# Performance work log

Measured on AMD Instinct MI355X. Metric: run time of the kernel, lower is better.

Reference implementation:

```python
import jax, jax.numpy as jnp
import numpy as np


def _gcn_norm(edge_index, edge_weight, n_nodes):
    # PyG gcn_norm with add_self_loops=True, fill_value=1.0.
    row, col = edge_index[0], edge_index[1]
    loop = jnp.arange(n_nodes, dtype=edge_index.dtype)
    row = jnp.concatenate([row, loop])
    col = jnp.concatenate([col, loop])
    w = jnp.concatenate([edge_weight, jnp.ones((n_nodes,), edge_weight.dtype)])
    deg = jax.ops.segment_sum(w, col, num_segments=n_nodes)
    dinv = jnp.where(deg > 0, jax.lax.rsqrt(deg), 0.0)
    norm = dinv[row] * w * dinv[col]
    return row, col, norm


def _gcn_conv(x, row, col, norm, W, b, n_nodes):
    h = x @ W                                  # [N, F_out]
    msg = h[row] * norm[:, None]               # gather + scale, [E+N, F_out]
    out = jax.ops.segment_sum(msg, col, num_segments=n_nodes)
    return out + b


def setup_inputs() -> dict:
    key = jax.random.key(0)
    k = jax.random.split(key, 7)
    N, E, Fin, Fout = 50000, 1600000, 256, 128
    H = 2 * Fout
    x = jax.random.normal(k[0], (N, Fin), dtype=jnp.float32)
    edge_index = jax.random.randint(k[1], (2, E), 0, N, dtype=jnp.int64)
    edge_weight = jax.random.uniform(k[2], (E,), dtype=jnp.float32)
    # Glorot init as in PyG GCNConv (weight stored as [in, out] here)
    s1 = float(np.sqrt(6.0 / (Fin + H)))
    s2 = float(np.sqrt(6.0 / (H + Fout)))
    W1 = jax.random.uniform(k[3], (Fin, H), minval=-s1, maxval=s1, dtype=jnp.float32)
    b1 = jnp.zeros((H,), jnp.float32)
    W2 = jax.random.uniform(k[4], (H, Fout), minval=-s2, maxval=s2, dtype=jnp.float32)
    b2 = jnp.zeros((Fout,), jnp.float32)
    return {"x": x, "edge_index": edge_index, "edge_weight": edge_weight,
            "W1": W1, "b1": b1, "W2": W2, "b2": b2}


def reference(x, edge_index, edge_weight, W1, b1, W2, b2):
    n_nodes = x.shape[0]
    # cached=True: normalization computed once, reused by both layers
    row, col, norm = _gcn_norm(edge_index, edge_weight, n_nodes)
    h = _gcn_conv(x, row, col, norm, W1, b1, n_nodes)
    h = jax.nn.relu(h)
    out = _gcn_conv(h, row, col, norm, W2, b2, n_nodes)
    return out
```

## Files before the change

### kernel.cpp

```cpp
#include <hip/hip_runtime.h>

typedef __attribute__((ext_vector_type(8))) short  short8;
typedef __attribute__((ext_vector_type(4))) float  f32x4;
typedef __attribute__((ext_vector_type(4))) ushort us4;
typedef __attribute__((ext_vector_type(4))) uint   u32x4;
typedef __attribute__((ext_vector_type(2))) uint   u32x2;
typedef unsigned long long ull;

__device__ __forceinline__ float bf2f(ushort u) {
    union { uint i; float f; } c; c.i = ((uint)u) << 16; return c.f;
}
__device__ __forceinline__ float bits2f(uint b) {
    union { uint i; float f; } c; c.i = b; return c.f;
}
__device__ __forceinline__ ushort f2bf(float f) {
    union { float f; uint i; } c; c.f = f;
    uint b = c.i + 0x7fffu + ((c.i >> 16) & 1u);
    return (ushort)(b >> 16);
}

#define NBLK  256
#define NBMAX 1024

__device__ __forceinline__
void histA_body(const int* __restrict__ col, int* __restrict__ counts,
                int E, int NB, uint* hist) {
    for (int j = threadIdx.x; j < NB; j += 256) hist[j] = 0u;
    __syncthreads();
    for (int i = blockIdx.x * 256 + threadIdx.x; i < E; i += 256 * NBLK)
        atomicAdd(&hist[((uint)col[i]) >> 6], 1u);
    __syncthreads();
    for (int j = threadIdx.x; j < NB; j += 256)
        counts[j * NBLK + blockIdx.x] = (int)hist[j];
}

__device__ __forceinline__
void binC_body(const int* __restrict__ row, const int* __restrict__ col,
               const float* __restrict__ w,
               const int* __restrict__ counts, const int* __restrict__ bbase,
               ull* __restrict__ recs, int E, int NB, uint* cur) {
    for (int j = threadIdx.x; j < NB; j += 256)
        cur[j] = (uint)(bbase[j] + counts[j * NBLK + blockIdx.x]);
    __syncthreads();
    for (int i = blockIdx.x * 256 + threadIdx.x; i < E; i += 256 * NBLK) {
        int c = col[i], r = row[i];
        float wv = w[i];
        uint w16 = (uint)(wv * 65536.0f);
        if (w16 > 65535u) w16 = 65535u;
        uint pos = atomicAdd(&cur[((uint)c) >> 6], 1u);
        recs[pos] = ((ull)(uint)c << 32) | (ull)((w16 << 16) | (uint)(r & 0xffff));
    }
}

__device__ __forceinline__
void binDa_body(const ull* __restrict__ recs, const int* __restrict__ bbase,
                int* __restrict__ cntp, float* __restrict__ dinv,
                int* __restrict__ btotP, int N,
                uint* cnt, uint* ws, uint* red) {
    int b = blockIdx.x, t = threadIdx.x;
    if (t < 64) { cnt[t] = 0u; ws[t] = 0u; }
    __syncthreads();
    int lo = bbase[b], hi = bbase[b + 1];
    for (int i = lo + t; i < hi; i += 256) {
        ull rec = recs[i];
        atomicAdd(&cnt[((uint)(rec >> 32)) & 63u], 1u);
        atomicAdd(&ws[((uint)(rec >> 32)) & 63u], (uint)((rec >> 16) & 0xffffu));
    }
    __syncthreads();
    uint cp = 0;
    if (t < 64) {
        int node = b * 64 + t;
        if (node < N) {
            cp = (cnt[t] + 3u) & ~3u;
            cntp[node] = (int)cp;
            dinv[node] = rsqrtf(1.0f + (float)ws[t] * (1.0f / 65536.0f));
        }
        red[t] = cp;
    }
    __syncthreads();
    if (t < 32) red[t] += red[t + 32];
    __syncthreads();
    if (t < 16) red[t] += red[t + 16];
    __syncthreads();
    if (t < 8) red[t] += red[t + 8];
    __syncthreads();
    if (t < 4) red[t] += red[t + 4];
    __syncthreads();
    if (t == 0) btotP[b] = (int)(red[0] + red[1] + red[2] + red[3]);
}

__device__ __forceinline__
void binDb_body(const ull* __restrict__ recs, const int* __restrict__ bbase,
                const int* __restrict__ bbaseP, const int* __restrict__ cntp,
                const float* __restrict__ dinv, int* __restrict__ rowptr,
                uint* __restrict__ edgesP, int N,
                uint* arr, uint* curN, uint* rbs) {
    int b = blockIdx.x, t = threadIdx.x;
    int node = b * 64 + t;
    uint cp = 0;
    if (t < 64 && node < N) cp = (uint)cntp[node];
    if (t < 64) arr[t] = cp;
    __syncthreads();
    for (int off = 1; off < 64; off <<= 1) {
        uint x = (t < 64 && t >= off) ? arr[t - off] : 0u;
        __syncthreads();
        if (t < 64) arr[t] += x;
        __syncthreads();
    }
    if (t < 64) {
        uint rb = (uint)bbaseP[b] + arr[t] - cp;
        rbs[t] = rb; curN[t] = rb;
        if (node < N) rowptr[node] = (int)rb;
    }
    __syncthreads();
    int lo = bbase[b], hi = bbase[b + 1];
    for (int i = lo + t; i < hi; i += 256) {
        ull rec = recs[i];
        uint c   = (uint)(rec >> 32);
        uint r   = (uint)rec & 0xffffu;
        uint w16 = ((uint)rec >> 16) & 0xffffu;
        float nv = dinv[r] * ((float)w16 * (1.0f / 65536.0f)) * dinv[c];
        uint slot = atomicAdd(&curN[c & 63u], 1u);
        edgesP[slot] = r | ((uint)f2bf(nv) << 16);
    }
    __syncthreads();
    if (t < 64 && node < N) {
        uint e1 = rbs[t] + cp;
        for (uint j = curN[t]; j < e1; ++j) edgesP[j] = 0u;
    }
}

__global__ void k_scanB1(int* __restrict__ counts, int* __restrict__ btot) {
    __shared__ int s[256];
    int b = blockIdx.x, t = threadIdx.x;
    int v = counts[b * NBLK + t];
    s[t] = v; __syncthreads();
    for (int off = 1; off < 256; off <<= 1) {
        int x = (t >= off) ? s[t - off] : 0;
        __syncthreads();
        s[t] += x;
        __syncthreads();
    }
    counts[b * NBLK + t] = s[t] - v;
    if (t == 255) btot[b] = s[255];
}

__global__ void k_scanB2(const int* __restrict__ btot, int* __restrict__ bbase, int NB) {
    __shared__ int s[256];
    int t = threadIdx.x;
    int v[4]; int sum = 0;
    #pragma unroll
    for (int j = 0; j < 4; ++j) {
        int i = t * 4 + j;
        v[j] = (i < NB) ? btot[i] : 0;
        sum += v[j];
    }
    s[t] = sum; __syncthreads();
    for (int off = 1; off < 256; off <<= 1) {
        int x = (t >= off) ? s[t - off] : 0;
        __syncthreads();
        s[t] += x;
        __syncthreads();
    }
    int excl = s[t] - sum;
    #pragma unroll
    for (int j = 0; j < 4; ++j) {
        int i = t * 4 + j;
        if (i <= NB) bbase[i] = excl;
        excl += v[j];
    }
}

__device__ __forceinline__
void splitT_body(const float* __restrict__ W, ushort* __restrict__ Th,
                 ushort* __restrict__ Tl, int K, int N, int i) {
    if (i < K * N) {
        int k = i / N, n = i - k * N;
        float v = W[i];
        ushort hi = f2bf(v);
        ushort lo = f2bf(v - bf2f(hi));
        Th[(size_t)n * K + k] = hi;
        Tl[(size_t)n * K + k] = lo;
    }
}

#define LDA 40

__device__ __forceinline__
void gemm3_body(const float* __restrict__ A, const ushort* __restrict__ BTh,
                const ushort* __restrict__ BTl, ushort* __restrict__ Cpan,
                int M, int Nc, int K, int bm, int bn,
                ushort (*As)[128][LDA], ushort (*Bs)[128][LDA]) {
    const int t    = threadIdx.x;
    const int lane = t & 63;
    const int wid  = t >> 6;
    const int wm   = wid >> 1;
    const int wn   = wid & 1;
    const int ml   = lane & 15;
    const int kq   = lane >> 4;

    f32x4 acc[4][4];
    #pragma unroll
    for (int mt = 0; mt < 4; ++mt)
        #pragma unroll
        for (int nt = 0; nt < 4; ++nt) acc[mt][nt] = (f32x4){0.f, 0.f, 0.f, 0.f};

    for (int k0 = 0; k0 < K; k0 += 32) {
        #pragma unroll
        for (int it = 0; it < 4; ++it) {
            int idx = (t + it * 256) * 4;
            int r  = idx >> 5;
            int kk = idx & 31;
            int grow = bm + r;
            f32x4 v = (f32x4){0.f, 0.f, 0.f, 0.f};
            if (grow < M) v = *(const f32x4*)&A[(size_t)grow * K + k0 + kk];
            us4 hi, lo;
            #pragma unroll
            for (int j = 0; j < 4; ++j) {
                ushort h = f2bf(v[j]);
                hi[j] = h;
                lo[j] = f2bf(v[j] - bf2f(h));
            }
            *(us4*)&As[0][r][kk] = hi;
            *(us4*)&As[1][r][kk] = lo;
        }
        #pragma unroll
        for (int it = 0; it < 2; ++it) {
            int idx = (t + it * 256) * 8;
            int n  = idx >> 5;
            int kk = idx & 31;
            u32x4 vh = *(const u32x4*)&BTh[(size_t)(bn + n) * K + k0 + kk];
            *(u32x4*)&Bs[0][n][kk] = vh;
            u32x4 vl = *(const u32x4*)&BTl[(size_t)(bn + n) * K + k0 + kk];
            *(u32x4*)&Bs[1][n][kk] = vl;
        }
        __syncthreads();

        short8 a[4][2], b[4][2];
        #pragma unroll
        for (int mt = 0; mt < 4; ++mt) {
            a[mt][0] = *(const short8*)&As[0][wm * 64 + mt * 16 + ml][kq * 8];
            a[mt][1] = *(const short8*)&As[1][wm * 64 + mt * 16 + ml][kq * 8];
        }
        #pragma unroll
        for (int nt = 0; nt < 4; ++nt) {
            b[nt][0] = *(const short8*)&Bs[0][wn * 64 + nt * 16 + ml][kq * 8];
            b[nt][1] = *(const short8*)&Bs[1][wn * 64 + nt * 16 + ml][kq * 8];
        }
        #pragma unroll
        for (int mt = 0; mt < 4; ++mt)
            #pragma unroll
            for (int nt = 0; nt < 4; ++nt) {
                acc[mt][nt] = __builtin_amdgcn_mfma_f32_16x16x32_bf16(a[mt][0], b[nt][0], acc[mt][nt], 0, 0, 0);
                acc[mt][nt] = __builtin_amdgcn_mfma_f32_16x16x32_bf16(a[mt][0], b[nt][1], acc[mt][nt], 0, 0, 0);
                acc[mt][nt] = __builtin_amdgcn_mfma_f32_16x16x32_bf16(a[mt][1], b[nt][0], acc[mt][nt], 0, 0, 0);
            }
        __syncthreads();
    }

    #pragma unroll
    for (int mt = 0; mt < 4; ++mt) {
        int rbase = bm + wm * 64 + mt * 16 + kq * 4;
        #pragma unroll
        for (int nt = 0; nt < 4; ++nt) {
            int colg = bn + wn * 64 + nt * 16 + ml;
            size_t pbase = (size_t)(colg >> 5) * M * 32 + (colg & 31);
            #pragma unroll
            for (int r = 0; r < 4; ++r) {
                int rr = rbase + r;
                if (rr < M) Cpan[pbase + (size_t)rr * 32] = f2bf(acc[mt][nt][r]);
            }
        }
    }
}

__global__ __launch_bounds__(256)
void k_gemm3(const float* __restrict__ A, const ushort* __restrict__ BTh,
             const ushort* __restrict__ BTl, ushort* __restrict__ Cpan,
             int M, int Nc, int K) {
    __shared__ __align__(16) ushort As[2][128][LDA];
    __shared__ __align__(16) ushort Bs[2][128][LDA];
    gemm3_body(A, BTh, BTl, Cpan, M, Nc, K, blockIdx.y * 128, blockIdx.x * 128, As, Bs);
}

__global__ __launch_bounds__(256)
void k_fusedA(const int* __restrict__ col, int* __restrict__ counts, int E, int NB,
              const float* __restrict__ W1, ushort* __restrict__ WT1h, ushort* __restrict__ WT1l,
              int Fin, int H,
              const float* __restrict__ W2, ushort* __restrict__ WT2h, ushort* __restrict__ WT2l,
              int Fout, int sp1) {
    __shared__ uint hist[NBMAX];
    int bid = (int)blockIdx.x;
    if (bid < NBLK) { histA_body(col, counts, E, NB, hist); return; }
    if (bid < NBLK + sp1) { splitT_body(W1, WT1h, WT1l, Fin, H, (bid - NBLK) * 256 + (int)threadIdx.x); return; }
    splitT_body(W2, WT2h, WT2l, H, Fout, (bid - NBLK - sp1) * 256 + (int)threadIdx.x);
}

__global__ __launch_bounds__(256)
void k_fusedB1(const int* __restrict__ row, const int* __restrict__ col,
               const float* __restrict__ w, const int* __restrict__ counts,
               const int* __restrict__ bbase, ull* __restrict__ recs, int E, int NB,
               const float* __restrict__ A, const ushort* __restrict__ BTh,
               const ushort* __restrict__ BTl, ushort* __restrict__ Cpan,
               int M, int Nc, int K, int t0) {
    __shared__ __align__(16) ushort As[2][128][LDA];
    __shared__ __align__(16) ushort Bs[2][128][LDA];
    int bid = (int)blockIdx.x;
    if (bid < NBLK) { binC_body(row, col, w, counts, bbase, recs, E, NB, (uint*)&As[0][0][0]); return; }
    int tile = t0 + bid - NBLK;
    int nbn = Nc >> 7;
    gemm3_body(A, BTh, BTl, Cpan, M, Nc, K, (tile / nbn) * 128, (tile % nbn) * 128, As, Bs);
}

__global__ __launch_bounds__(256)
void k_fusedB2(const ull* __restrict__ recs, const int* __restrict__ bbase,
               int* __restrict__ cntp, float* __restrict__ dinv, int* __restrict__ btotP,
               int N, int NB,
               const float* __restrict__ A, const ushort* __restrict__ BTh,
               const ushort* __restrict__ BTl, ushort* __restrict__ Cpan,
               int M, int Nc, int K, int t0) {
    __shared__ __align__(16) ushort As[2][128][LDA];
    __shared__ __align__(16) ushort Bs[2][128][LDA];
    int bid = (int)blockIdx.x;
    if (bid < NB) {
        uint* l = (uint*)&As[0][0][0];
        binDa_body(recs, bbase, cntp, dinv, btotP, N, l, l + 64, l + 128);
        return;
    }
    int tile = t0 + bid - NB;
    int nbn = Nc >> 7;
    gemm3_body(A, BTh, BTl, Cpan, M, Nc, K, (tile / nbn) * 128, (tile % nbn) * 128, As, Bs);
}

__global__ __launch_bounds__(256)
void k_fusedB3(const ull* __restrict__ recs, const int* __restrict__ bbase,
               const int* __restrict__ bbaseP, const int* __restrict__ cntp,
               const float* __restrict__ dinv, int* __restrict__ rowptr,
               uint* __restrict__ edgesP, int N, int NB,
               const float* __restrict__ A, const ushort* __restrict__ BTh,
               const ushort* __restrict__ BTl, ushort* __restrict__ Cpan,
               int M, int Nc, int K, int t0) {
    __shared__ __align__(16) ushort As[2][128][LDA];
    __shared__ __align__(16) ushort Bs[2][128][LDA];
    int bid = (int)blockIdx.x;
    if (bid < NB) {
        uint* l = (uint*)&As[0][0][0];
        binDb_body(recs, bbase, bbaseP, cntp, dinv, rowptr, edgesP, N, l, l + 64, l + 128);
        return;
    }
    int tile = t0 + bid - NB;
    int nbn = Nc >> 7;
    gemm3_body(A, BTh, BTl, Cpan, M, Nc, K, (tile / nbn) * 128, (tile % nbn) * 128, As, Bs);
}

#define NPB 64

template <bool RELU>
__device__ __forceinline__
void aggr_body(const int* __restrict__ rowptr, const int* __restrict__ cntp,
               const uint* __restrict__ edges,
               const ushort* __restrict__ hpan, const float* __restrict__ dinv,
               const float* __restrict__ bias, float* __restrict__ out,
               int F, int npan, int N) {
    const int bid  = blockIdx.x;
    const int p    = bid % npan;
    const int wave = threadIdx.x >> 6;
    const int lane = threadIdx.x & 63;
    const int g    = lane >> 2;
    const int c    = lane & 3;
    const int node = (bid / npan) * NPB + wave * 16 + g;
    const int fbase = p * 32 + c * 8;

    const ushort* hp = hpan + (size_t)p * N * 32 + c * 8;

    int beg = 0, end = 0;
    if (node < N) { beg = rowptr[node]; end = beg + cntp[node]; }

    float acc[8] = {};
    int e = beg;
    u32x4 pk4 = (u32x4){0u, 0u, 0u, 0u};
    if (e < end) pk4 = *(const u32x4*)&edges[e];
    while (__any(e < end)) {
        u32x4 cur = pk4;
        int e2 = e + 4;
        if (e2 < end) pk4 = *(const u32x4*)&edges[e2];
        if (e < end) {
            #pragma unroll
            for (int j = 0; j < 4; ++j) {
                uint pk = cur[j];
                float nv = bits2f(pk & 0xffff0000u);
                int r = (int)(pk & 0xffffu);
                u32x4 hv = *(const u32x4*)(hp + (size_t)r * 32);
                #pragma unroll
                for (int q = 0; q < 4; ++q) {
                    acc[2 * q]     += nv * bits2f(hv[q] << 16);
                    acc[2 * q + 1] += nv * bits2f(hv[q] & 0xffff0000u);
                }
            }
        }
        e = e2;
    }

    if (node < N) {
        float di = dinv[node];
        float d2 = di * di;
        u32x4 hs = *(const u32x4*)(hp + (size_t)node * 32);
        f32x4 bv0 = *(const f32x4*)&bias[fbase];
        f32x4 bv1 = *(const f32x4*)&bias[fbase + 4];
        f32x4 v0, v1;
        #pragma unroll
        for (int q = 0; q < 4; ++q) {
            float r0 = acc[2 * q]     + d2 * bits2f(hs[q] << 16)
                     + ((q < 2) ? bv0[2 * q] : bv1[2 * q - 4]);
            float r1 = acc[2 * q + 1] + d2 * bits2f(hs[q] & 0xffff0000u)
                     + ((q < 2) ? bv0[2 * q + 1] : bv1[2 * q - 3]);
            if (RELU) { r0 = fmaxf(r0, 0.f); r1 = fmaxf(r1, 0.f); }
            if (q < 2) { v0[2 * q] = r0; v0[2 * q + 1] = r1; }
            else       { v1[2 * q - 4] = r0; v1[2 * q - 3] = r1; }
        }
        *(f32x4*)&out[(size_t)node * F + fbase]     = v0;
        *(f32x4*)&out[(size_t)node * F + fbase + 4] = v1;
    }
}

__global__ __launch_bounds__(256)
void k_aggr1(const int* __restrict__ rowptr, const int* __restrict__ cntp,
             const uint* __restrict__ edges, const ushort* __restrict__ hpan,
             const float* __restrict__ dinv, const float* __restrict__ bias,
             float* __restrict__ out, int F, int npan, int N) {
    aggr_body<true>(rowptr, cntp, edges, hpan, dinv, bias, out, F, npan, N);
}

__global__ __launch_bounds__(256)
void k_aggr2(const int* __restrict__ rowptr, const int* __restrict__ cntp,
             const uint* __restrict__ edges, const ushort* __restrict__ hpan,
             const float* __restrict__ dinv, const float* __restrict__ bias,
             float* __restrict__ out, int F, int npan, int N) {
    aggr_body<false>(rowptr, cntp, edges, hpan, dinv, bias, out, F, npan, N);
}


static inline char* bump(char*& p, size_t bytes) {
    char* r = p;
    p += (bytes + 255) & ~(size_t)255;
    return r;
}

extern "C" void kernel_launch(void* const* d_in, const int* in_sizes, int n_in,
                              void* d_out, int out_size, void* d_ws, size_t ws_size,
                              hipStream_t stream) {
    const float* x  = (const float*)d_in[0];
    const int*   ei = (const int*)d_in[1];
    const float* ew = (const float*)d_in[2];
    const float* W1 = (const float*)d_in[3];
    const float* b1 = (const float*)d_in[4];
    const float* W2 = (const float*)d_in[5];
    const float* b2 = (const float*)d_in[6];
    float* out = (float*)d_out;

    const int E    = in_sizes[2];
    const int H    = in_sizes[4];
    const int Fout = in_sizes[6];
    const int Fin  = in_sizes[3] / H;
    const int N    = in_sizes[0] / Fin;
    const int NB   = (N + 63) >> 6;

    const int* row = ei;
    const int* col = ei + E;

    char* p = (char*)d_ws;
    float*  dinv   = (float*)bump(p, (size_t)N * 4);
    int*    cntp   = (int*)bump(p, (size_t)N * 4);
    int*    rowptr = (int*)bump(p, (size_t)N * 4);
    uint*   edgesP = (uint*)bump(p, ((size_t)E + 4 * N + 256) * 4);
    int*    counts = (int*)bump(p, (size_t)NBMAX * NBLK * 4);
    int*    btot   = (int*)bump(p, (size_t)NBMAX * 4);
    int*    bbase  = (int*)bump(p, (size_t)(NBMAX + 1) * 4);
    int*    btotP  = (int*)bump(p, (size_t)NBMAX * 4);
    int*    bbaseP = (int*)bump(p, (size_t)(NBMAX + 1) * 4);
    ushort* WT1h   = (ushort*)bump(p, (size_t)Fin * H * 2);
    ushort* WT1l   = (ushort*)bump(p, (size_t)Fin * H * 2);
    ushort* WT2h   = (ushort*)bump(p, (size_t)H * Fout * 2);
    ushort* WT2l   = (ushort*)bump(p, (size_t)H * Fout * 2);
    ushort* h1     = (ushort*)bump(p, (size_t)N * H * 2);
    float*  a1     = (float*)bump(p, (size_t)N * H * 4);
    ushort* h2     = (ushort*)bump(p, (size_t)N * Fout * 2);

    ull* recs = (ull*)a1;

    const int sp1 = (Fin * H + 255) / 256;
    const int sp2 = (H * Fout + 255) / 256;
    const int gb1 = (H / 128) * ((N + 127) / 128);
    int T1 = gb1 < 280 ? gb1 : 280;
    int T2 = gb1 < 480 ? gb1 : 480;
    if (T2 < T1) T2 = T1;

    k_fusedA<<<NBLK + sp1 + sp2, 256, 0, stream>>>(col, counts, E, NB,
                                                   W1, WT1h, WT1l, Fin, H,
                                                   W2, WT2h, WT2l, Fout, sp1);
    k_scanB1<<<NB, 256, 0, stream>>>(counts, btot);
    k_scanB2<<<1, 256, 0, stream>>>(btot, bbase, NB);
    k_fusedB1<<<NBLK + T1, 256, 0, stream>>>(row, col, ew, counts, bbase, recs, E, NB,
                                             x, WT1h, WT1l, h1, N, H, Fin, 0);
    k_fusedB2<<<NB + (T2 - T1), 256, 0, stream>>>(recs, bbase, cntp, dinv, btotP, N, NB,
                                                  x, WT1h, WT1l, h1, N, H, Fin, T1);
    k_scanB2<<<1, 256, 0, stream>>>(btotP, bbaseP, NB);
    k_fusedB3<<<NB + (gb1 - T2), 256, 0, stream>>>(recs, bbase, bbaseP, cntp, dinv,
                                                   rowptr, edgesP, N, NB,
                                                   x, WT1h, WT1l, h1, N, H, Fin, T2);

    const int chunks = (N + NPB - 1) / NPB;

    k_aggr1<<<chunks * (H / 32), 256, 0, stream>>>(rowptr, cntp, edgesP, h1, dinv, b1, a1, H, H / 32, N);

    k_gemm3<<<dim3(Fout / 128, (N + 127) / 128), 256, 0, stream>>>(a1, WT2h, WT2l, h2, N, Fout, H);
    k_aggr2<<<chunks * (Fout / 32), 256, 0, stream>>>(rowptr, cntp, edgesP, h2, dinv, b2, out, Fout, Fout / 32, N);
}
```

Baseline: 417.5 us.

## Sort nodes by padded degree for aggregation and drop second per-bin scan

Builds a counting sort of nodes by padded in-degree bucket (histogram, scan, placement into a ushort perm array) and has both aggregation kernels walk nodes in that order. Nodes sharing a wave then have similar edge counts, which cuts divergence and idle lanes. Row pointers are now computed in the degree pass from a fixed per-bin over-allocation (192 slots per bin), so the second block-total scan launch goes away. The cost is extra atomics, a small scan kernel, scattered output writes and lost locality between neighbouring nodes, and the perm indices are limited to 16 bits.

After: 890.1 us. 113% more time.

```diff
diff --git a/kernel.cpp b/kernel.cpp
--- a/kernel.cpp
+++ b/kernel.cpp
@@ -55,8 +55,8 @@
 __device__ __forceinline__
 void binDa_body(const ull* __restrict__ recs, const int* __restrict__ bbase,
                 int* __restrict__ cntp, float* __restrict__ dinv,
-                int* __restrict__ btotP, int N,
-                uint* cnt, uint* ws, uint* red) {
+                int* __restrict__ rowptr, uint* __restrict__ pkhist, int N,
+                uint* cnt, uint* ws, uint* arr) {
     int b = blockIdx.x, t = threadIdx.x;
     if (t < 64) { cnt[t] = 0u; ws[t] = 0u; }
     __syncthreads();
@@ -67,50 +67,41 @@
         atomicAdd(&ws[((uint)(rec >> 32)) & 63u], (uint)((rec >> 16) & 0xffffu));
     }
     __syncthreads();
+    int node = b * 64 + t;
     uint cp = 0;
     if (t < 64) {
-        int node = b * 64 + t;
-        if (node < N) {
-            cp = (cnt[t] + 3u) & ~3u;
-            cntp[node] = (int)cp;
-            dinv[node] = rsqrtf(1.0f + (float)ws[t] * (1.0f / 65536.0f));
-        }
-        red[t] = cp;
-    }
-    __syncthreads();
-    if (t < 32) red[t] += red[t + 32];
-    __syncthreads();
-    if (t < 16) red[t] += red[t + 16];
-    __syncthreads();
-    if (t < 8) red[t] += red[t + 8];
-    __syncthreads();
-    if (t < 4) red[t] += red[t + 4];
-    __syncthreads();
-    if (t == 0) btotP[b] = (int)(red[0] + red[1] + red[2] + red[3]);
+        if (node < N) cp = (cnt[t] + 3u) & ~3u;
+        arr[t] = cp;
+    }
+    __syncthreads();
+    for (int off = 1; off < 64; off <<= 1) {
+        uint x = (t < 64 && t >= off) ? arr[t - off] : 0u;
+        __syncthreads();
+        if (t < 64) arr[t] += x;
+        __syncthreads();
+    }
+    if (t < 64 && node < N) {
+        int base = bbase[b] + 192 * b;
+        rowptr[node] = base + (int)(arr[t] - cp);
+        cntp[node]   = (int)cp;
+        dinv[node]   = rsqrtf(1.0f + (float)ws[t] * (1.0f / 65536.0f));
+        uint key = cp >> 2;
+        if (key > 63u) key = 63u;
+        atomicAdd(&pkhist[key], 1u);
+    }
 }
 
 __device__ __forceinline__
 void binDb_body(const ull* __restrict__ recs, const int* __restrict__ bbase,
-                const int* __restrict__ bbaseP, const int* __restrict__ cntp,
-                const float* __restrict__ dinv, int* __restrict__ rowptr,
-                uint* __restrict__ edgesP, int N,
-                uint* arr, uint* curN, uint* rbs) {
+                const int* __restrict__ rowptr, const int* __restrict__ cntp,
+                const float* __restrict__ dinv, uint* __restrict__ edgesP, int N,
+                uint* curN, uint* rbs, uint* cps) {
     int b = blockIdx.x, t = threadIdx.x;
     int node = b * 64 + t;
-    uint cp = 0;
-    if (t < 64 && node < N) cp = (uint)cntp[node];
-    if (t < 64) arr[t] = cp;
-    __syncthreads();
-    for (int off = 1; off < 64; off <<= 1) {
-        uint x = (t < 64 && t >= off) ? arr[t - off] : 0u;
-        __syncthreads();
-        if (t < 64) arr[t] += x;
-        __syncthreads();
-    }
     if (t < 64) {
-        uint rb = (uint)bbaseP[b] + arr[t] - cp;
-        rbs[t] = rb; curN[t] = rb;
-        if (node < N) rowptr[node] = (int)rb;
+        uint rp = 0u, cp = 0u;
+        if (node < N) { rp = (uint)rowptr[node]; cp = (uint)cntp[node]; }
+        rbs[t] = rp; curN[t] = rp; cps[t] = cp;
     }
     __syncthreads();
     int lo = bbase[b], hi = bbase[b + 1];
@@ -125,8 +116,20 @@
     }
     __syncthreads();
     if (t < 64 && node < N) {
-        uint e1 = rbs[t] + cp;
+        uint e1 = rbs[t] + cps[t];
         for (uint j = curN[t]; j < e1; ++j) edgesP[j] = 0u;
+    }
+}
+
+__device__ __forceinline__
+void permPlace_body(const int* __restrict__ cntp, uint* __restrict__ pkbase,
+                    ushort* __restrict__ perm, int N, int blk) {
+    int i = blk * 256 + (int)threadIdx.x;
+    if (i < N) {
+        uint key = ((uint)cntp[i]) >> 2;
+        if (key > 63u) key = 63u;
+        uint pos = atomicAdd(&pkbase[key], 1u);
+        perm[pos] = (ushort)i;
     }
 }
 
@@ -145,9 +148,11 @@
     if (t == 255) btot[b] = s[255];
 }
 
-__global__ void k_scanB2(const int* __restrict__ btot, int* __restrict__ bbase, int NB) {
+__global__ void k_scanB2(const int* __restrict__ btot, int* __restrict__ bbase,
+                         int NB, uint* __restrict__ pkhist) {
     __shared__ int s[256];
     int t = threadIdx.x;
+    if (t < 64) pkhist[t] = 0u;
     int v[4]; int sum = 0;
     #pragma unroll
     for (int j = 0; j < 4; ++j) {
@@ -169,6 +174,20 @@
         if (i <= NB) bbase[i] = excl;
         excl += v[j];
     }
+}
+
+__global__ void k_permScan(const uint* __restrict__ pkhist, uint* __restrict__ pkbase) {
+    __shared__ uint s[64];
+    int t = threadIdx.x;
+    uint v = pkhist[t];
+    s[t] = v; __syncthreads();
+    for (int off = 1; off < 64; off <<= 1) {
+        uint x = (t >= off) ? s[t - off] : 0u;
+        __syncthreads();
+        s[t] += x;
+        __syncthreads();
+    }
+    pkbase[t] = s[t] - v;
 }
 
 __device__ __forceinline__
@@ -314,7 +333,8 @@
 
 __global__ __launch_bounds__(256)
 void k_fusedB2(const ull* __restrict__ recs, const int* __restrict__ bbase,
-               int* __restrict__ cntp, float* __restrict__ dinv, int* __restrict__ btotP,
+               int* __restrict__ cntp, float* __restrict__ dinv,
+               int* __restrict__ rowptr, uint* __restrict__ pkhist,
                int N, int NB,
                const float* __restrict__ A, const ushort* __restrict__ BTh,
                const ushort* __restrict__ BTl, ushort* __restrict__ Cpan,
@@ -324,7 +344,7 @@
     int bid = (int)blockIdx.x;
     if (bid < NB) {
         uint* l = (uint*)&As[0][0][0];
-        binDa_body(recs, bbase, cntp, dinv, btotP, N, l, l + 64, l + 128);
+        binDa_body(recs, bbase, cntp, dinv, rowptr, pkhist, N, l, l + 64, l + 128);
         return;
     }
     int tile = t0 + bid - NB;
@@ -334,9 +354,10 @@
 
 __global__ __launch_bounds__(256)
 void k_fusedB3(const ull* __restrict__ recs, const int* __restrict__ bbase,
-               const int* __restrict__ bbaseP, const int* __restrict__ cntp,
-               const float* __restrict__ dinv, int* __restrict__ rowptr,
-               uint* __restrict__ edgesP, int N, int NB,
+               const int* __restrict__ rowptr, const int* __restrict__ cntp,
+               const float* __restrict__ dinv, uint* __restrict__ edgesP,
+               uint* __restrict__ pkbase, ushort* __restrict__ perm,
+               int N, int NB, int pp,
                const float* __restrict__ A, const ushort* __restrict__ BTh,
                const ushort* __restrict__ BTl, ushort* __restrict__ Cpan,
                int M, int Nc, int K, int t0) {
@@ -345,10 +366,11 @@
     int bid = (int)blockIdx.x;
     if (bid < NB) {
         uint* l = (uint*)&As[0][0][0];
-        binDb_body(recs, bbase, bbaseP, cntp, dinv, rowptr, edgesP, N, l, l + 64, l + 128);
+        binDb_body(recs, bbase, rowptr, cntp, dinv, edgesP, N, l, l + 64, l + 128);
         return;
     }
-    int tile = t0 + bid - NB;
+    if (bid < NB + pp) { permPlace_body(cntp, pkbase, perm, N, bid - NB); return; }
+    int tile = t0 + bid - NB - pp;
     int nbn = Nc >> 7;
     gemm3_body(A, BTh, BTl, Cpan, M, Nc, K, (tile / nbn) * 128, (tile % nbn) * 128, As, Bs);
 }
@@ -357,8 +379,8 @@
 
 template <bool RELU>
 __device__ __forceinline__
-void aggr_body(const int* __restrict__ rowptr, const int* __restrict__ cntp,
-               const uint* __restrict__ edges,
+void aggr_body(const ushort* __restrict__ perm, const int* __restrict__ rowptr,
+               const int* __restrict__ cntp, const uint* __restrict__ edges,
                const ushort* __restrict__ hpan, const float* __restrict__ dinv,
                const float* __restrict__ bias, float* __restrict__ out,
                int F, int npan, int N) {
@@ -368,13 +390,17 @@
     const int lane = threadIdx.x & 63;
     const int g    = lane >> 2;
     const int c    = lane & 3;
-    const int node = (bid / npan) * NPB + wave * 16 + g;
+    const int idx  = (bid / npan) * NPB + wave * 16 + g;
     const int fbase = p * 32 + c * 8;
 
     const ushort* hp = hpan + (size_t)p * N * 32 + c * 8;
 
-    int beg = 0, end = 0;
-    if (node < N) { beg = rowptr[node]; end = beg + cntp[node]; }
+    int node = 0, beg = 0, end = 0;
+    if (idx < N) {
+        node = (int)perm[idx];
+        beg = rowptr[node];
+        end = beg + cntp[node];
+    }
 
     float acc[8] = {};
     int e = beg;
@@ -401,7 +427,7 @@
         e = e2;
     }
 
-    if (node < N) {
+    if (idx < N) {
         float di = dinv[node];
         float d2 = di * di;
         u32x4 hs = *(const u32x4*)(hp + (size_t)node * 32);
@@ -424,19 +450,21 @@
 }
 
 __global__ __launch_bounds__(256)
-void k_aggr1(const int* __restrict__ rowptr, const int* __restrict__ cntp,
-             const uint* __restrict__ edges, const ushort* __restrict__ hpan,
-             const float* __restrict__ dinv, const float* __restrict__ bias,
-             float* __restrict__ out, int F, int npan, int N) {
-    aggr_body<true>(rowptr, cntp, edges, hpan, dinv, bias, out, F, npan, N);
-}
-
-__global__ __launch_bounds__(256)
-void k_aggr2(const int* __restrict__ rowptr, const int* __restrict__ cntp,
-             const uint* __restrict__ edges, const ushort* __restrict__ hpan,
-             const float* __restrict__ dinv, const float* __restrict__ bias,
-             float* __restrict__ out, int F, int npan, int N) {
-    aggr_body<false>(rowptr, cntp, edges, hpan, dinv, bias, out, F, npan, N);
+void k_aggr1(const ushort* __restrict__ perm, const int* __restrict__ rowptr,
+             const int* __restrict__ cntp, const uint* __restrict__ edges,
+             const ushort* __restrict__ hpan, const float* __restrict__ dinv,
+             const float* __restrict__ bias, float* __restrict__ out,
+             int F, int npan, int N) {
+    aggr_body<true>(perm, rowptr, cntp, edges, hpan, dinv, bias, out, F, npan, N);
+}
+
+__global__ __launch_bounds__(256)
+void k_aggr2(const ushort* __restrict__ perm, const int* __restrict__ rowptr,
+             const int* __restrict__ cntp, const uint* __restrict__ edges,
+             const ushort* __restrict__ hpan, const float* __restrict__ dinv,
+             const float* __restrict__ bias, float* __restrict__ out,
+             int F, int npan, int N) {
+    aggr_body<false>(perm, rowptr, cntp, edges, hpan, dinv, bias, out, F, npan, N);
 }
 
 
@@ -472,12 +500,13 @@
     float*  dinv   = (float*)bump(p, (size_t)N * 4);
     int*    cntp   = (int*)bump(p, (size_t)N * 4);
     int*    rowptr = (int*)bump(p, (size_t)N * 4);
-    uint*   edgesP = (uint*)bump(p, ((size_t)E + 4 * N + 256) * 4);
+    ushort* perm   = (ushort*)bump(p, (size_t)N * 2);
+    uint*   pkhist = (uint*)bump(p, 64 * 4);
+    uint*   pkbase = (uint*)bump(p, 64 * 4);
+    uint*   edgesP = (uint*)bump(p, ((size_t)E + 3 * N + 192 * (size_t)NBMAX + 256) * 4);
     int*    counts = (int*)bump(p, (size_t)NBMAX * NBLK * 4);
     int*    btot   = (int*)bump(p, (size_t)NBMAX * 4);
     int*    bbase  = (int*)bump(p, (size_t)(NBMAX + 1) * 4);
-    int*    btotP  = (int*)bump(p, (size_t)NBMAX * 4);
-    int*    bbaseP = (int*)bump(p, (size_t)(NBMAX + 1) * 4);
     ushort* WT1h   = (ushort*)bump(p, (size_t)Fin * H * 2);
     ushort* WT1l   = (ushort*)bump(p, (size_t)Fin * H * 2);
     ushort* WT2h   = (ushort*)bump(p, (size_t)H * Fout * 2);
@@ -491,6 +520,7 @@
     const int sp1 = (Fin * H + 255) / 256;
     const int sp2 = (H * Fout + 255) / 256;
     const int gb1 = (H / 128) * ((N + 127) / 128);
+    const int pp  = (N + 255) / 256;
     int T1 = gb1 < 280 ? gb1 : 280;
     int T2 = gb1 < 480 ? gb1 : 480;
     if (T2 < T1) T2 = T1;
@@ -499,20 +529,20 @@
                                                    W1, WT1h, WT1l, Fin, H,
                                                    W2, WT2h, WT2l, Fout, sp1);
     k_scanB1<<<NB, 256, 0, stream>>>(counts, btot);
-    k_scanB2<<<1, 256, 0, stream>>>(btot, bbase, NB);
+    k_scanB2<<<1, 256, 0, stream>>>(btot, bbase, NB, pkhist);
     k_fusedB1<<<NBLK + T1, 256, 0, stream>>>(row, col, ew, counts, bbase, recs, E, NB,
                                              x, WT1h, WT1l, h1, N, H, Fin, 0);
-    k_fusedB2<<<NB + (T2 - T1), 256, 0, stream>>>(recs, bbase, cntp, dinv, btotP, N, NB,
-                                                  x, WT1h, WT1l, h1, N, H, Fin, T1);
-    k_scanB2<<<1, 256, 0, stream>>>(btotP, bbaseP, NB);
-    k_fusedB3<<<NB + (gb1 - T2), 256, 0, stream>>>(recs, bbase, bbaseP, cntp, dinv,
-                                                   rowptr, edgesP, N, NB,
-                                                   x, WT1h, WT1l, h1, N, H, Fin, T2);
+    k_fusedB2<<<NB + (T2 - T1), 256, 0, stream>>>(recs, bbase, cntp, dinv, rowptr, pkhist,
+                                                  N, NB, x, WT1h, WT1l, h1, N, H, Fin, T1);
+    k_permScan<<<1, 64, 0, stream>>>(pkhist, pkbase);
+    k_fusedB3<<<NB + pp + (gb1 - T2), 256, 0, stream>>>(recs, bbase, rowptr, cntp, dinv,
+                                                        edgesP, pkbase, perm, N, NB, pp,
+                                                        x, WT1h, WT1l, h1, N, H, Fin, T2);
 
     const int chunks = (N + NPB - 1) / NPB;
 
-    k_aggr1<<<chunks * (H / 32), 256, 0, stream>>>(rowptr, cntp, edgesP, h1, dinv, b1, a1, H, H / 32, N);
+    k_aggr1<<<chunks * (H / 32), 256, 0, stream>>>(perm, rowptr, cntp, edgesP, h1, dinv, b1, a1, H, H / 32, N);
 
     k_gemm3<<<dim3(Fout / 128, (N + 127) / 128), 256, 0, stream>>>(a1, WT2h, WT2l, h2, N, Fout, H);
-    k_aggr2<<<chunks * (Fout / 32), 256, 0, stream>>>(rowptr, cntp, edgesP, h2, dinv, b2, out, Fout, Fout / 32, N);
-}
+    k_aggr2<<<chunks * (Fout / 32), 256, 0, stream>>>(perm, rowptr, cntp, edgesP, h2, dinv, b2, out, Fout, Fout / 32, N);
+}
```
